# Optimization experiments

Hardware: AMD Instinct MI355X
Metric: run time of the kernel (lower is better)

The kernel has to match this reference:

```python
import jax, jax.numpy as jnp
import numpy as np

KDIM = 8192
EPS = 1e-8  # F.cosine_similarity default eps


def _encoder(x, W1, b1, W2, b2, W3, b3):
    # x: [..., KDIM] -> [..., 128]; Linear(KDIM,512)->ReLU->Linear(512,256)->ReLU->Linear(256,128)
    h = jax.nn.relu(x @ W1 + b1)
    h = jax.nn.relu(h @ W2 + b2)
    return h @ W3 + b3


def setup_inputs() -> dict:
    key = jax.random.key(0)
    ks = jax.random.split(key, 16)

    def lin(k, fan_in, fan_out):
        bound = 1.0 / np.sqrt(fan_in)
        kw, kb = jax.random.split(k)
        W = jax.random.uniform(kw, (fan_in, fan_out), jnp.float32, -bound, bound)
        b = jax.random.uniform(kb, (fan_out,), jnp.float32, -bound, bound)
        return W, b

    W1, b1 = lin(ks[0], KDIM, 512)
    W2, b2 = lin(ks[1], 512, 256)
    W3, b3 = lin(ks[2], 256, 128)
    Wi1, bi1 = lin(ks[3], 128 + 6, 64)
    Wi2, bi2 = lin(ks[4], 64, 32)
    Wi3, bi3 = lin(ks[5], 32, 1)

    return {
        "new_knowledge": jax.random.normal(ks[6], (KDIM,), jnp.float32),
        "existing_knowledge": jax.random.normal(ks[7], (10, KDIM), jnp.float32),
        "math_metrics": jax.random.uniform(ks[8], (6,), jnp.float32),
        "W1": W1, "b1": b1, "W2": W2, "b2": b2, "W3": W3, "b3": b3,
        "Wi1": Wi1, "bi1": bi1, "Wi2": Wi2, "bi2": bi2, "Wi3": Wi3, "bi3": bi3,
    }


def reference(new_knowledge, existing_knowledge, math_metrics,
              W1, b1, W2, b2, W3, b3, Wi1, bi1, Wi2, bi2, Wi3, bi3):
    # Encode new knowledge: [128]
    new_enc = _encoder(new_knowledge, W1, b1, W2, b2, W3, b3)
    # Batched encode of the (up to 10) existing knowledge vectors: [10, 128]
    ex_enc = _encoder(existing_knowledge, W1, b1, W2, b2, W3, b3)

    # Per-item geometric distance (L2 norm of difference)
    diff = new_enc[None, :] - ex_enc                     # [10, 128]
    geo_dist = jnp.sqrt(jnp.sum(diff * diff, axis=-1))   # [10]

    # Per-item cosine similarity with torch eps clamping
    new_n = jnp.maximum(jnp.linalg.norm(new_enc), EPS)
    ex_n = jnp.maximum(jnp.linalg.norm(ex_enc, axis=-1), EPS)  # [10]
    cos = (ex_enc @ new_enc) / (new_n * ex_n)            # [10]

    avg_consistency = jnp.mean(geo_dist - cos)

    # Mathematical-constraint integrator MLP on [128 + 6]
    combined = jnp.concatenate([new_enc, math_metrics])  # [134]
    h = jax.nn.relu(combined @ Wi1 + bi1)
    h = jax.nn.relu(h @ Wi2 + bi2)
    quality = h @ Wi3 + bi3                              # [1]

    integration_loss = jnp.exp(-quality)                 # [1]
    total = jnp.squeeze(avg_consistency + integration_loss)
    return total
```

## Files before the change

kernel.cpp:

```cpp
#include <hip/hip_runtime.h>
#include <math.h>

#define EPS 1e-8f

__device__ __forceinline__ float wredsum(float v) {
#pragma unroll
  for (int o = 32; o > 0; o >>= 1) v += __shfl_down(v, o, 64);
  return v;
}

__global__ __launch_bounds__(256) void k_l1(const float* __restrict__ xn,
                                            const float* __restrict__ xe,
                                            const float* __restrict__ W1,
                                            float* __restrict__ p1) {
  __shared__ float red[11 * 16 * 65];
  const int cg  = threadIdx.x & 15;
  const int ks  = threadIdx.x >> 4;
  const int col = blockIdx.x * 64 + cg * 4;
  const int k0  = blockIdx.y * 256 + ks * 16;

  float4 acc[11];
#pragma unroll
  for (int r = 0; r < 11; ++r) acc[r] = make_float4(0.f, 0.f, 0.f, 0.f);

#pragma unroll 8
  for (int i = 0; i < 16; ++i) {
    const int k = k0 + i;
    const float4 w = *(const float4*)&W1[(size_t)k * 512 + col];
    float xv = xn[k];
    acc[0].x = fmaf(xv, w.x, acc[0].x); acc[0].y = fmaf(xv, w.y, acc[0].y);
    acc[0].z = fmaf(xv, w.z, acc[0].z); acc[0].w = fmaf(xv, w.w, acc[0].w);
#pragma unroll
    for (int r = 0; r < 10; ++r) {
      const float xr = xe[r * 8192 + k];
      acc[r + 1].x = fmaf(xr, w.x, acc[r + 1].x);
      acc[r + 1].y = fmaf(xr, w.y, acc[r + 1].y);
      acc[r + 1].z = fmaf(xr, w.z, acc[r + 1].z);
      acc[r + 1].w = fmaf(xr, w.w, acc[r + 1].w);
    }
  }

#pragma unroll
  for (int r = 0; r < 11; ++r) {
    const int base = (r * 16 + ks) * 65 + cg * 4;
    red[base]     = acc[r].x; red[base + 1] = acc[r].y;
    red[base + 2] = acc[r].z; red[base + 3] = acc[r].w;
  }
  __syncthreads();
  if (threadIdx.x < 176) {
    const int r = threadIdx.x >> 4;
    const int c = threadIdx.x & 15;
    float4 s = make_float4(0.f, 0.f, 0.f, 0.f);
#pragma unroll
    for (int k = 0; k < 16; ++k) {
      const int b = (r * 16 + k) * 65 + c * 4;
      s.x += red[b]; s.y += red[b + 1]; s.z += red[b + 2]; s.w += red[b + 3];
    }
    *(float4*)&p1[((size_t)blockIdx.y * 11 + r) * 512 + blockIdx.x * 64 + c * 4] = s;
  }
}

__global__ __launch_bounds__(256) void k_h1(const float* __restrict__ p1,
                                            const float* __restrict__ b1,
                                            float* __restrict__ H1) {
  const int idx = blockIdx.x * 256 + threadIdx.x;
  float s = 0.f;
#pragma unroll
  for (int ch = 0; ch < 32; ++ch) s += p1[(size_t)ch * 5632 + idx];
  H1[idx] = fmaxf(s + b1[idx & 511], 0.f);
}

__global__ __launch_bounds__(256) void k_h2(const float* __restrict__ H1,
                                            const float* __restrict__ W2,
                                            const float* __restrict__ b2,
                                            float* __restrict__ H2) {
  __shared__ float h1s[5632];
  __shared__ float red[11 * 16 * 17];
  const int tid = threadIdx.x;
  for (int i = tid; i < 1408; i += 256)
    *(float4*)&h1s[i * 4] = *(const float4*)&H1[i * 4];
  __syncthreads();

  const int c = tid & 15, ks = tid >> 4;
  const int col = blockIdx.x * 16 + c;
  float acc[11];
#pragma unroll
  for (int r = 0; r < 11; ++r) acc[r] = 0.f;
#pragma unroll
  for (int kk = 0; kk < 32; ++kk) {
    const int k = kk * 16 + ks;
    const float wv = W2[(size_t)k * 256 + col];
#pragma unroll
    for (int r = 0; r < 11; ++r) acc[r] = fmaf(h1s[r * 512 + k], wv, acc[r]);
  }
#pragma unroll
  for (int r = 0; r < 11; ++r) red[(r * 16 + ks) * 17 + c] = acc[r];
  __syncthreads();
  if (tid < 176) {
    const int r = tid >> 4, cc = tid & 15;
    float s = 0.f;
#pragma unroll
    for (int k = 0; k < 16; ++k) s += red[(r * 16 + k) * 17 + cc];
    const int oc = blockIdx.x * 16 + cc;
    H2[r * 256 + oc] = fmaxf(s + b2[oc], 0.f);
  }
}

__global__ __launch_bounds__(1024) void k_fin(
    const float* __restrict__ H2, const float* __restrict__ W3,
    const float* __restrict__ b3, const float* __restrict__ mm,
    const float* __restrict__ Wi1, const float* __restrict__ bi1,
    const float* __restrict__ Wi2, const float* __restrict__ bi2,
    const float* __restrict__ Wi3, const float* __restrict__ bi3,
    float* __restrict__ out) {
  __shared__ __align__(16) float h2s[2816];
  __shared__ __align__(16) float wi1s[8576];
  __shared__ float red[11 * 8 * 128];
  __shared__ float encs[1408];
  __shared__ float comb[134];
  __shared__ float h1s[64];
  const int t = threadIdx.x;

  for (int i = t; i < 2848; i += 1024) {
    if (i < 704) *(float4*)&h2s[i * 4] = *(const float4*)&H2[i * 4];
    else         *(float4*)&wi1s[(i - 704) * 4] = *(const float4*)&Wi1[(size_t)(i - 704) * 4];
  }
  __syncthreads();

  {
    const int c = t & 127, g = t >> 7;
    float acc[11];
#pragma unroll
    for (int r = 0; r < 11; ++r) acc[r] = 0.f;
#pragma unroll
    for (int kk = 0; kk < 32; ++kk) {
      const int k = g * 32 + kk;
      const float wv = W3[(size_t)k * 128 + c];
#pragma unroll
      for (int r = 0; r < 11; ++r) acc[r] = fmaf(h2s[r * 256 + k], wv, acc[r]);
    }
#pragma unroll
    for (int r = 0; r < 11; ++r) red[(r * 8 + g) * 128 + c] = acc[r];
  }
  __syncthreads();
  for (int o = t; o < 1408; o += 1024) {
    const int r = o >> 7, c = o & 127;
    float s = b3[c];
#pragma unroll
    for (int g = 0; g < 8; ++g) s += red[(r * 8 + g) * 128 + c];
    encs[o] = s;
  }
  __syncthreads();

  float consist = 0.f;
  float n0 = 0.f, n1 = 0.f;
  if (t < 64) {
    n0 = encs[t]; n1 = encs[64 + t];
    comb[t] = n0; comb[64 + t] = n1;
    if (t < 6) comb[128 + t] = mm[t];
  }
  __syncthreads();
  if (t < 64) {
    const float nn = wredsum(n0 * n0 + n1 * n1);
#pragma unroll
    for (int r = 1; r <= 10; ++r) {
      const float e0 = encs[r * 128 + t];
      const float e1 = encs[r * 128 + 64 + t];
      const float d0 = e0 - n0, d1 = e1 - n1;
      const float g  = wredsum(d0 * d0 + d1 * d1);
      const float q  = wredsum(e0 * e0 + e1 * e1);
      const float dd = wredsum(e0 * n0 + e1 * n1);
      if (t == 0) {
        const float geo = sqrtf(g);
        const float den = fmaxf(sqrtf(nn), EPS) * fmaxf(sqrtf(q), EPS);
        consist += geo - dd / den;
      }
    }
  } else if (t < 128) {
    const int tt = t - 64;
    float h = bi1[tt];
#pragma unroll 4
    for (int k = 0; k < 134; ++k) h = fmaf(comb[k], wi1s[k * 64 + tt], h);
    h1s[tt] = fmaxf(h, 0.f);
  }
  __syncthreads();
  if (t < 64) {
    float part = 0.f;
    if (t < 32) {
      float h2 = bi2[t];
#pragma unroll 8
      for (int k = 0; k < 64; ++k) h2 = fmaf(h1s[k], Wi2[k * 32 + t], h2);
      part = fmaxf(h2, 0.f) * Wi3[t];
    }
    const float qual = wredsum(part);
    if (t == 0) out[0] = consist * 0.1f + expf(-(qual + bi3[0]));
  }
}

extern "C" void kernel_launch(void* const* d_in, const int* in_sizes, int n_in,
                              void* d_out, int out_size, void* d_ws, size_t ws_size,
                              hipStream_t stream) {
  (void)in_sizes; (void)n_in; (void)out_size; (void)ws_size;
  const float* xn  = (const float*)d_in[0];
  const float* xe  = (const float*)d_in[1];
  const float* mm  = (const float*)d_in[2];
  const float* W1  = (const float*)d_in[3];
  const float* b1  = (const float*)d_in[4];
  const float* W2  = (const float*)d_in[5];
  const float* b2  = (const float*)d_in[6];
  const float* W3  = (const float*)d_in[7];
  const float* b3  = (const float*)d_in[8];
  const float* Wi1 = (const float*)d_in[9];
  const float* bi1 = (const float*)d_in[10];
  const float* Wi2 = (const float*)d_in[11];
  const float* bi2 = (const float*)d_in[12];
  const float* Wi3 = (const float*)d_in[13];
  const float* bi3 = (const float*)d_in[14];
  float* out = (float*)d_out;

  char* ws = (char*)d_ws;
  float* p1 = (float*)(ws);
  float* H1 = (float*)(ws + 720896);
  float* H2 = (float*)(ws + 743424);

  hipLaunchKernelGGL(k_l1,  dim3(8, 32), dim3(256),  0, stream, xn, xe, W1, p1);
  hipLaunchKernelGGL(k_h1,  dim3(22),    dim3(256),  0, stream, p1, b1, H1);
  hipLaunchKernelGGL(k_h2,  dim3(16),    dim3(256),  0, stream, H1, W2, b2, H2);
  hipLaunchKernelGGL(k_fin, dim3(1),     dim3(1024), 0, stream,
                     H2, W3, b3, mm, Wi1, bi1, Wi2, bi2, Wi3, bi3, out);
}
```

Before: 120.6 us.

## Fuse layer-1 reduction, layer 2 and tail into one last-block-wins kernel

Merges the H1 reduction, the second linear layer and the final encoder/integrator kernel into one 8-block launch. Each block reduces its 64-column slice of layer-1 partials, computes a partial layer-2 product over that K slice, and writes it to a workspace. An atomic counter picks the last block to arrive, which sums the partials and runs the rest of the tail. This removes two kernel launches and their inter-kernel gaps, at the cost of a global atomic handshake and an extra partial-sum buffer.

```diff
diff --git a/kernel.cpp b/kernel.cpp
--- a/kernel.cpp
+++ b/kernel.cpp
@@ -12,7 +12,9 @@
 __global__ __launch_bounds__(256) void k_l1(const float* __restrict__ xn,
                                             const float* __restrict__ xe,
                                             const float* __restrict__ W1,
-                                            float* __restrict__ p1) {
+                                            float* __restrict__ p1,
+                                            int* __restrict__ bars) {
+  if (blockIdx.x == 0 && blockIdx.y == 0 && threadIdx.x == 0) bars[0] = 0;
   __shared__ float red[11 * 16 * 65];
   const int cg  = threadIdx.x & 15;
   const int ks  = threadIdx.x >> 4;
@@ -60,70 +62,76 @@
   }
 }
 
-__global__ __launch_bounds__(256) void k_h1(const float* __restrict__ p1,
-                                            const float* __restrict__ b1,
-                                            float* __restrict__ H1) {
-  const int idx = blockIdx.x * 256 + threadIdx.x;
-  float s = 0.f;
-#pragma unroll
-  for (int ch = 0; ch < 32; ++ch) s += p1[(size_t)ch * 5632 + idx];
-  H1[idx] = fmaxf(s + b1[idx & 511], 0.f);
-}
-
-__global__ __launch_bounds__(256) void k_h2(const float* __restrict__ H1,
-                                            const float* __restrict__ W2,
-                                            const float* __restrict__ b2,
-                                            float* __restrict__ H2) {
-  __shared__ float h1s[5632];
-  __shared__ float red[11 * 16 * 17];
-  const int tid = threadIdx.x;
-  for (int i = tid; i < 1408; i += 256)
-    *(float4*)&h1s[i * 4] = *(const float4*)&H1[i * 4];
-  __syncthreads();
-
-  const int c = tid & 15, ks = tid >> 4;
-  const int col = blockIdx.x * 16 + c;
-  float acc[11];
-#pragma unroll
-  for (int r = 0; r < 11; ++r) acc[r] = 0.f;
-#pragma unroll
-  for (int kk = 0; kk < 32; ++kk) {
-    const int k = kk * 16 + ks;
-    const float wv = W2[(size_t)k * 256 + col];
-#pragma unroll
-    for (int r = 0; r < 11; ++r) acc[r] = fmaf(h1s[r * 512 + k], wv, acc[r]);
-  }
-#pragma unroll
-  for (int r = 0; r < 11; ++r) red[(r * 16 + ks) * 17 + c] = acc[r];
-  __syncthreads();
-  if (tid < 176) {
-    const int r = tid >> 4, cc = tid & 15;
-    float s = 0.f;
-#pragma unroll
-    for (int k = 0; k < 16; ++k) s += red[(r * 16 + k) * 17 + cc];
-    const int oc = blockIdx.x * 16 + cc;
-    H2[r * 256 + oc] = fmaxf(s + b2[oc], 0.f);
-  }
-}
-
-__global__ __launch_bounds__(1024) void k_fin(
-    const float* __restrict__ H2, const float* __restrict__ W3,
-    const float* __restrict__ b3, const float* __restrict__ mm,
+__global__ __launch_bounds__(1024) void k_tail(
+    const float* __restrict__ p1, const float* __restrict__ b1,
+    const float* __restrict__ W2, const float* __restrict__ b2,
+    const float* __restrict__ W3, const float* __restrict__ b3,
+    const float* __restrict__ mm,
     const float* __restrict__ Wi1, const float* __restrict__ bi1,
     const float* __restrict__ Wi2, const float* __restrict__ bi2,
     const float* __restrict__ Wi3, const float* __restrict__ bi3,
-    float* __restrict__ out) {
-  __shared__ __align__(16) float h2s[2816];
-  __shared__ __align__(16) float wi1s[8576];
-  __shared__ float red[11 * 8 * 128];
+    float* __restrict__ p2, int* __restrict__ bars, float* __restrict__ out) {
+  __shared__ float h1sl[11 * 64];
+  __shared__ float red[11264];
+  __shared__ float h2s[11 * 256];
+  __shared__ __align__(16) float wi1s[134 * 64];
   __shared__ float encs[1408];
   __shared__ float comb[134];
-  __shared__ float h1s[64];
+  __shared__ float h1b[64];
+  __shared__ int won;
   const int t = threadIdx.x;
-
-  for (int i = t; i < 2848; i += 1024) {
-    if (i < 704) *(float4*)&h2s[i * 4] = *(const float4*)&H2[i * 4];
-    else         *(float4*)&wi1s[(i - 704) * 4] = *(const float4*)&Wi1[(size_t)(i - 704) * 4];
+  const int j = blockIdx.x;
+
+  if (t < 704) {
+    const int r = t >> 6, kk = t & 63;
+    const int col = j * 64 + kk;
+    float s = b1[col];
+#pragma unroll
+    for (int ch = 0; ch < 32; ++ch) s += p1[(size_t)ch * 5632 + r * 512 + col];
+    h1sl[r * 64 + kk] = fmaxf(s, 0.f);
+  }
+  __syncthreads();
+
+  {
+    const int col = t & 255, g = t >> 8;
+    float acc[11];
+#pragma unroll
+    for (int r = 0; r < 11; ++r) acc[r] = 0.f;
+#pragma unroll
+    for (int kk = 0; kk < 16; ++kk) {
+      const int kl = g * 16 + kk;
+      const float w = W2[(size_t)(j * 64 + kl) * 256 + col];
+#pragma unroll
+      for (int r = 0; r < 11; ++r) acc[r] = fmaf(h1sl[r * 64 + kl], w, acc[r]);
+    }
+#pragma unroll
+    for (int r = 0; r < 11; ++r) red[(g * 11 + r) * 256 + col] = acc[r];
+  }
+  __syncthreads();
+  for (int o = t; o < 2816; o += 1024) {
+    const int col = o & 255, r = o >> 8;
+    p2[j * 2816 + o] = red[r * 256 + col] + red[(11 + r) * 256 + col] +
+                       red[(22 + r) * 256 + col] + red[(33 + r) * 256 + col];
+  }
+
+  __syncthreads();
+  if (t == 0) {
+    __threadfence();
+    const int old = __hip_atomic_fetch_add(bars, 1, __ATOMIC_ACQ_REL,
+                                           __HIP_MEMORY_SCOPE_AGENT);
+    won = (old == 7);
+    if (won) __threadfence();
+  }
+  __syncthreads();
+  if (!won) return;
+
+  for (int i = t; i < 2144; i += 1024)
+    *(float4*)&wi1s[i * 4] = *(const float4*)&Wi1[(size_t)i * 4];
+  for (int o = t; o < 2816; o += 1024) {
+    float s = b2[o & 255];
+#pragma unroll
+    for (int jj = 0; jj < 8; ++jj) s += p2[jj * 2816 + o];
+    h2s[o] = fmaxf(s, 0.f);
   }
   __syncthreads();
 
@@ -135,19 +143,19 @@
 #pragma unroll
     for (int kk = 0; kk < 32; ++kk) {
       const int k = g * 32 + kk;
-      const float wv = W3[(size_t)k * 128 + c];
-#pragma unroll
-      for (int r = 0; r < 11; ++r) acc[r] = fmaf(h2s[r * 256 + k], wv, acc[r]);
-    }
-#pragma unroll
-    for (int r = 0; r < 11; ++r) red[(r * 8 + g) * 128 + c] = acc[r];
+      const float w = W3[(size_t)k * 128 + c];
+#pragma unroll
+      for (int r = 0; r < 11; ++r) acc[r] = fmaf(h2s[r * 256 + k], w, acc[r]);
+    }
+#pragma unroll
+    for (int r = 0; r < 11; ++r) red[(g * 11 + r) * 128 + c] = acc[r];
   }
   __syncthreads();
   for (int o = t; o < 1408; o += 1024) {
-    const int r = o >> 7, c = o & 127;
+    const int c = o & 127, r = o >> 7;
     float s = b3[c];
 #pragma unroll
-    for (int g = 0; g < 8; ++g) s += red[(r * 8 + g) * 128 + c];
+    for (int g = 0; g < 8; ++g) s += red[(g * 11 + r) * 128 + c];
     encs[o] = s;
   }
   __syncthreads();
@@ -181,7 +189,7 @@
     float h = bi1[tt];
 #pragma unroll 4
     for (int k = 0; k < 134; ++k) h = fmaf(comb[k], wi1s[k * 64 + tt], h);
-    h1s[tt] = fmaxf(h, 0.f);
+    h1b[tt] = fmaxf(h, 0.f);
   }
   __syncthreads();
   if (t < 64) {
@@ -189,7 +197,7 @@
     if (t < 32) {
       float h2 = bi2[t];
 #pragma unroll 8
-      for (int k = 0; k < 64; ++k) h2 = fmaf(h1s[k], Wi2[k * 32 + t], h2);
+      for (int k = 0; k < 64; ++k) h2 = fmaf(h1b[k], Wi2[k * 32 + t], h2);
       part = fmaxf(h2, 0.f) * Wi3[t];
     }
     const float qual = wredsum(part);
@@ -219,13 +227,12 @@
   float* out = (float*)d_out;
 
   char* ws = (char*)d_ws;
-  float* p1 = (float*)(ws);
-  float* H1 = (float*)(ws + 720896);
-  float* H2 = (float*)(ws + 743424);
-
-  hipLaunchKernelGGL(k_l1,  dim3(8, 32), dim3(256),  0, stream, xn, xe, W1, p1);
-  hipLaunchKernelGGL(k_h1,  dim3(22),    dim3(256),  0, stream, p1, b1, H1);
-  hipLaunchKernelGGL(k_h2,  dim3(16),    dim3(256),  0, stream, H1, W2, b2, H2);
-  hipLaunchKernelGGL(k_fin, dim3(1),     dim3(1024), 0, stream,
-                     H2, W3, b3, mm, Wi1, bi1, Wi2, bi2, Wi3, bi3, out);
-}
+  float* p1   = (float*)(ws);
+  float* p2   = (float*)(ws + 720896);
+  int*   bars = (int*)  (ws + 811008);
+
+  hipLaunchKernelGGL(k_l1,   dim3(8, 32), dim3(256),  0, stream, xn, xe, W1, p1, bars);
+  hipLaunchKernelGGL(k_tail, dim3(8),     dim3(1024), 0, stream,
+                     p1, b1, W2, b2, W3, b3, mm,
+                     Wi1, bi1, Wi2, bi2, Wi3, bi3, p2, bars, out);
+}
```

After: 120.5 us. No clear change (-0.1%).
